# Performance work log

Hardware: AMD Instinct MI355X
Metric: run time of the kernel (lower is better)

Reference implementation:

```python
import math
import jax, jax.numpy as jnp
import numpy as np

B, S, D, H = 4, 2048, 1024, 16
HD = D // H
EPS = 1e-5
NEG = 1e10


def setup_inputs() -> dict:
    key = jax.random.key(0)
    ks = jax.random.split(key, 6)
    std = 0.02
    return {
        "x": jax.random.normal(ks[0], (B, S, D), dtype=jnp.float32),
        "ln1_w": jnp.ones((D,), jnp.float32),
        "ln1_b": jnp.zeros((D,), jnp.float32),
        "W_attn": jax.random.normal(ks[1], (D, 3 * D), jnp.float32) * std,
        "b_attn": jnp.zeros((3 * D,), jnp.float32),
        "W_cproj": jax.random.normal(ks[2], (D, D), jnp.float32) * std,
        "b_cproj": jnp.zeros((D,), jnp.float32),
        "ln2_w": jnp.ones((D,), jnp.float32),
        "ln2_b": jnp.zeros((D,), jnp.float32),
        "W_fc": jax.random.normal(ks[3], (D, 4 * D), jnp.float32) * std,
        "b_fc": jnp.zeros((4 * D,), jnp.float32),
        "W_mproj": jax.random.normal(ks[4], (4 * D, D), jnp.float32) * std,
        "b_mproj": jnp.zeros((D,), jnp.float32),
    }


def _layernorm(x, w, b):
    u = jnp.mean(x, axis=-1, keepdims=True)
    s = jnp.mean((x - u) ** 2, axis=-1, keepdims=True)
    return w * ((x - u) / jnp.sqrt(s + EPS)) + b


def _gelu(x):
    return 0.5 * x * (1 + jnp.tanh(math.sqrt(2 / math.pi) * (x + 0.044715 * x ** 3)))


def _block(x, ln1_w, ln1_b, W_attn, b_attn, W_cproj, b_cproj,
           ln2_w, ln2_b, W_fc, b_fc, W_mproj, b_mproj):
    h = _layernorm(x, ln1_w, ln1_b)
    qkv = h @ W_attn + b_attn                       # [B,S,3D]
    q, k, v = jnp.split(qkv, 3, axis=-1)
    # split heads -> [B,H,S,hd]
    q = q.reshape(B, S, H, HD).transpose(0, 2, 1, 3)
    k = k.reshape(B, S, H, HD).transpose(0, 2, 1, 3)
    v = v.reshape(B, S, H, HD).transpose(0, 2, 1, 3)
    w = jnp.einsum('bhqd,bhkd->bhqk', q, k) / math.sqrt(HD)
    bias = jnp.tril(jnp.ones((S, S), jnp.float32))  # causal mask
    w = w * bias - NEG * (1 - bias)
    w = jax.nn.softmax(w, axis=-1)
    a = jnp.einsum('bhqk,bhkd->bhqd', w, v)
    a = a.transpose(0, 2, 1, 3).reshape(B, S, D)    # merge heads
    a = a @ W_cproj + b_cproj
    x = x + a                                        # residual
    m = _layernorm(x, ln2_w, ln2_b)
    m = _gelu(m @ W_fc + b_fc) @ W_mproj + b_mproj
    return x + m


def reference(x, ln1_w, ln1_b, W_attn, b_attn, W_cproj, b_cproj,
              ln2_w, ln2_b, W_fc, b_fc, W_mproj, b_mproj):
    return _block(x, ln1_w, ln1_b, W_attn, b_attn, W_cproj, b_cproj,
                  ln2_w, ln2_b, W_fc, b_fc, W_mproj, b_mproj)
```

## Files before the change

### kernel.cpp

```cpp
#include <hip/hip_runtime.h>
#include <hip/hip_bf16.h>
#include <math.h>


typedef __attribute__((ext_vector_type(8))) short short8;
typedef __attribute__((ext_vector_type(4))) float floatx4;

#define MFMA16(a, b, c) __builtin_amdgcn_mfma_f32_16x16x32_bf16((a), (b), (c), 0, 0, 0)

__device__ __forceinline__ short f2bf(float f) {
    union { float f; unsigned u; } a; a.f = f;
    unsigned r = a.u + 0x7fffu + ((a.u >> 16) & 1u);
    return (short)(r >> 16);
}

__device__ __forceinline__ float fexp2(float x) {
    return exp2f(x);
}

__device__ __forceinline__ float gelu_f(float x) {
    return 0.5f * x * (1.0f + tanhf(0.7978845608028654f * (x + 0.044715f * x * x * x)));
}

__device__ __forceinline__ void gload_lds16(const short* g, short* l) {
    __builtin_amdgcn_global_load_lds((const __attribute__((address_space(1))) void*)g,
                                     (__attribute__((address_space(3))) void*)l, 16, 0, 0);
}

__global__ void tcast_kernel(const float* __restrict__ W, short* __restrict__ Wt,
                             int K, int N) {
    __shared__ float tile[32][33];
    const int bx = blockIdx.x * 32;
    const int by = blockIdx.y * 32;
    const int tx = threadIdx.x;
    const int ty = threadIdx.y;
#pragma unroll
    for (int i = 0; i < 32; i += 8)
        tile[ty + i][tx] = W[(size_t)(by + ty + i) * N + bx + tx];
    __syncthreads();
#pragma unroll
    for (int i = 0; i < 32; i += 8)
        Wt[(size_t)(bx + ty + i) * K + by + tx] = f2bf(tile[tx][ty + i]);
}

__global__ __launch_bounds__(256) void ln_kernel(const float* __restrict__ x,
                                                 const float* __restrict__ w,
                                                 const float* __restrict__ b,
                                                 short* __restrict__ out) {
    const int row = blockIdx.x;
    const int t = threadIdx.x;
    const float4 v = ((const float4*)(x + (size_t)row * 1024))[t];
    float s = v.x + v.y + v.z + v.w;
    float s2 = v.x * v.x + v.y * v.y + v.z * v.z + v.w * v.w;
#pragma unroll
    for (int d = 32; d >= 1; d >>= 1) {
        s += __shfl_xor(s, d, 64);
        s2 += __shfl_xor(s2, d, 64);
    }
    __shared__ float red[8];
    const int wid = t >> 6, lane = t & 63;
    if (lane == 0) { red[wid * 2] = s; red[wid * 2 + 1] = s2; }
    __syncthreads();
    s = red[0] + red[2] + red[4] + red[6];
    s2 = red[1] + red[3] + red[5] + red[7];
    const float mean = s * (1.f / 1024.f);
    const float var = s2 * (1.f / 1024.f) - mean * mean;
    const float rstd = rsqrtf(var + 1e-5f);
    const float4 wv = ((const float4*)w)[t];
    const float4 bv = ((const float4*)b)[t];
    union { ushort4 u; short sa[4]; } ov;
    ov.sa[0] = f2bf(wv.x * ((v.x - mean) * rstd) + bv.x);
    ov.sa[1] = f2bf(wv.y * ((v.y - mean) * rstd) + bv.y);
    ov.sa[2] = f2bf(wv.z * ((v.z - mean) * rstd) + bv.z);
    ov.sa[3] = f2bf(wv.w * ((v.w - mean) * rstd) + bv.w);
    ((ushort4*)(out + (size_t)row * 1024))[t] = ov.u;
}

template <int EPI>
__global__ __launch_bounds__(256) void gemm_kernel(
    const short* __restrict__ A, const short* __restrict__ Bt,
    const float* __restrict__ bias, const float* __restrict__ res,
    void* __restrict__ Cout, int M, int N, int K) {
    __shared__ __align__(16) short As[128][32];
    __shared__ __align__(16) short Bs[128][32];

    const int tid = threadIdx.x;
    const int wid = tid >> 6;
    const int lane = tid & 63;
    const int quad = lane >> 4;
    const int l16 = lane & 15;
    const int wm = (wid >> 1) * 64;
    const int wn = (wid & 1) * 64;
    const int m0 = blockIdx.y * 128;
    const int n0 = blockIdx.x * 128;

    const int lr = lane >> 2;
    const int lc = (lane & 3) * 8;

    floatx4 acc[4][4] = {};

    const short* ga0 = A + (size_t)(m0 + wid * 16 + lr) * K + lc;
    const short* ga1 = A + (size_t)(m0 + 64 + wid * 16 + lr) * K + lc;
    const short* gb0 = Bt + (size_t)(n0 + wid * 16 + lr) * K + lc;
    const short* gb1 = Bt + (size_t)(n0 + 64 + wid * 16 + lr) * K + lc;
    short* lA0 = &As[wid * 16][0];
    short* lA1 = &As[64 + wid * 16][0];
    short* lB0 = &Bs[wid * 16][0];
    short* lB1 = &Bs[64 + wid * 16][0];

    for (int k0 = 0; k0 < K; k0 += 32) {
        gload_lds16(ga0 + k0, lA0);
        gload_lds16(ga1 + k0, lA1);
        gload_lds16(gb0 + k0, lB0);
        gload_lds16(gb1 + k0, lB1);
        __syncthreads();
        short8 af[4], bf[4];
#pragma unroll
        for (int mt = 0; mt < 4; mt++)
            af[mt] = *(const short8*)&As[wm + mt * 16 + l16][quad * 8];
#pragma unroll
        for (int nt = 0; nt < 4; nt++)
            bf[nt] = *(const short8*)&Bs[wn + nt * 16 + l16][quad * 8];
#pragma unroll
        for (int mt = 0; mt < 4; mt++)
#pragma unroll
            for (int nt = 0; nt < 4; nt++)
                acc[mt][nt] = MFMA16(af[mt], bf[nt], acc[mt][nt]);
        __syncthreads();
    }
#pragma unroll
    for (int nt = 0; nt < 4; nt++) {
        const int col = n0 + wn + nt * 16 + l16;
        const float bv = bias[col];
#pragma unroll
        for (int mt = 0; mt < 4; mt++) {
#pragma unroll
            for (int r = 0; r < 4; r++) {
                const int row = m0 + wm + mt * 16 + quad * 4 + r;
                const size_t idx = (size_t)row * N + col;
                float v = acc[mt][nt][r] + bv;
                if constexpr (EPI == 0) {
                    ((short*)Cout)[idx] = f2bf(v);
                } else if constexpr (EPI == 1) {
                    ((short*)Cout)[idx] = f2bf(gelu_f(v));
                } else {
                    ((float*)Cout)[idx] = v + res[idx];
                }
            }
        }
    }
}

__global__ __launch_bounds__(256) void attn_kernel(const short* __restrict__ qkv,
                                                   short* __restrict__ aout) {
    __shared__ __align__(16) short smem[9216];
    short* Ks = smem;
    short* Vs = smem + 64 * 72;

    const int tid = threadIdx.x;
    const int wid = tid >> 6;
    const int lane = tid & 63;
    const int quad = lane >> 4;
    const int l16 = lane & 15;

    const int qtile = 15 - blockIdx.y;
    const int q0 = qtile * 128;
    const int bh = blockIdx.x;
    const int b = bh >> 4;
    const int h = bh & 15;

    const short* base = qkv + (size_t)b * 2048 * 3072 + h * 64;
    const int qrow_base = q0 + wid * 32;

    short8 qf[2][2];
#pragma unroll
    for (int qt = 0; qt < 2; qt++)
#pragma unroll
        for (int ks = 0; ks < 2; ks++)
            qf[qt][ks] = *(const short8*)(base +
                (size_t)(qrow_base + qt * 16 + l16) * 3072 + ks * 32 + quad * 8);

    floatx4 o[4][2] = {};
    float mrow[2] = {-1e30f, -1e30f};
    float lrow[2] = {0.f, 0.f};
    const float SCL = 0.125f * 1.44269504f;

    const int nkt = qtile * 2 + 2;
    for (int kt = 0; kt < nkt; kt++) {
        const int kt0 = kt * 64;
        {
            const int r = tid >> 2;
            const int cg = (tid & 3) * 16;
            const short* krow = base + (size_t)(kt0 + r) * 3072 + 1024 + cg;
            const short* vrow = base + (size_t)(kt0 + r) * 3072 + 2048 + cg;
            *(uint4*)&Ks[r * 72 + cg] = ((const uint4*)krow)[0];
            *(uint4*)&Ks[r * 72 + cg + 8] = ((const uint4*)krow)[1];
            *(uint2*)&Vs[r * 68 + cg] = ((const uint2*)vrow)[0];
            *(uint2*)&Vs[r * 68 + cg + 4] = ((const uint2*)vrow)[1];
            *(uint2*)&Vs[r * 68 + cg + 8] = ((const uint2*)vrow)[2];
            *(uint2*)&Vs[r * 68 + cg + 12] = ((const uint2*)vrow)[3];
        }
        __syncthreads();
        if (kt0 <= qrow_base + 31) {
            floatx4 st[4][2] = {};
#pragma unroll
            for (int kti = 0; kti < 4; kti++) {
                const short8 kf0 = *(const short8*)&Ks[(kti * 16 + l16) * 72 + quad * 8];
                const short8 kf1 = *(const short8*)&Ks[(kti * 16 + l16) * 72 + 32 + quad * 8];
#pragma unroll
                for (int qt = 0; qt < 2; qt++) {
                    st[kti][qt] = MFMA16(kf0, qf[qt][0], st[kti][qt]);
                    st[kti][qt] = MFMA16(kf1, qf[qt][1], st[kti][qt]);
                }
            }
            const bool needmask = (kt0 + 63) > qrow_base;
            short8 pk[2][2];
#pragma unroll
            for (int qt = 0; qt < 2; qt++) {
                const int q = qrow_base + qt * 16 + l16;
#pragma unroll
                for (int kti = 0; kti < 4; kti++)
#pragma unroll
                    for (int r = 0; r < 4; r++) {
                        float v = st[kti][qt][r] * SCL;
                        if (needmask && (kt0 + kti * 16 + quad * 4 + r) > q) v = -1e30f;
                        st[kti][qt][r] = v;
                    }
                float mx = -1e30f;
#pragma unroll
                for (int kti = 0; kti < 4; kti++)
#pragma unroll
                    for (int r = 0; r < 4; r++) mx = fmaxf(mx, st[kti][qt][r]);
                mx = fmaxf(mx, __shfl_xor(mx, 16, 64));
                mx = fmaxf(mx, __shfl_xor(mx, 32, 64));
                const float mnew = fmaxf(mrow[qt], mx);
                const float alpha = fexp2(mrow[qt] - mnew);
                mrow[qt] = mnew;
                float ps = 0.f;
#pragma unroll
                for (int kti = 0; kti < 4; kti++)
#pragma unroll
                    for (int r = 0; r < 4; r++) {
                        const float p = fexp2(st[kti][qt][r] - mnew);
                        st[kti][qt][r] = p;
                        ps += p;
                    }
                ps += __shfl_xor(ps, 16, 64);
                ps += __shfl_xor(ps, 32, 64);
                lrow[qt] = lrow[qt] * alpha + ps;
#pragma unroll
                for (int dt = 0; dt < 4; dt++) o[dt][qt] *= alpha;
#pragma unroll
                for (int kti = 0; kti < 4; kti++)
#pragma unroll
                    for (int r = 0; r < 4; r++)
                        pk[kti >> 1][qt][(kti & 1) * 4 + r] = f2bf(st[kti][qt][r]);
            }
#pragma unroll
            for (int c = 0; c < 2; c++)
#pragma unroll
                for (int dt = 0; dt < 4; dt++) {
                    short8 vf;
#pragma unroll
                    for (int j = 0; j < 4; j++) {
                        vf[j]     = Vs[(c * 32 + quad * 4 + j) * 68 + dt * 16 + l16];
                        vf[4 + j] = Vs[(c * 32 + 16 + quad * 4 + j) * 68 + dt * 16 + l16];
                    }
                    o[dt][0] = MFMA16(vf, pk[c][0], o[dt][0]);
                    o[dt][1] = MFMA16(vf, pk[c][1], o[dt][1]);
                }
        }
        __syncthreads();
    }
    short* Ow = smem + wid * (32 * 72);
    const float rl0 = 1.0f / lrow[0];
    const float rl1 = 1.0f / lrow[1];
#pragma unroll
    for (int dt = 0; dt < 4; dt++)
#pragma unroll
        for (int r = 0; r < 4; r++) {
            Ow[(l16) * 72 + dt * 16 + quad * 4 + r] = f2bf(o[dt][0][r] * rl0);
            Ow[(16 + l16) * 72 + dt * 16 + quad * 4 + r] = f2bf(o[dt][1][r] * rl1);
        }
    __asm__ volatile("s_waitcnt lgkmcnt(0)" ::: "memory");
    {
        const int ql = lane >> 1;
        const int h2 = lane & 1;
        short* orow = aout + (size_t)(b * 2048 + q0 + wid * 32 + ql) * 1024 + h * 64 + h2 * 32;
#pragma unroll
        for (int s = 0; s < 4; s++)
            *(uint4*)(orow + s * 8) = *(const uint4*)&Ow[ql * 72 + h2 * 32 + s * 8];
    }
}

extern "C" void kernel_launch(void* const* d_in, const int* in_sizes, int n_in,
                              void* d_out, int out_size, void* d_ws, size_t ws_size,
                              hipStream_t stream) {
    const float* x       = (const float*)d_in[0];
    const float* ln1_w   = (const float*)d_in[1];
    const float* ln1_b   = (const float*)d_in[2];
    const float* W_attn  = (const float*)d_in[3];
    const float* b_attn  = (const float*)d_in[4];
    const float* W_cproj = (const float*)d_in[5];
    const float* b_cproj = (const float*)d_in[6];
    const float* ln2_w   = (const float*)d_in[7];
    const float* ln2_b   = (const float*)d_in[8];
    const float* W_fc    = (const float*)d_in[9];
    const float* b_fc    = (const float*)d_in[10];
    const float* W_mproj = (const float*)d_in[11];
    const float* b_mproj = (const float*)d_in[12];

    char* ws = (char*)d_ws;
    short* W1t  = (short*)(ws + 0);
    short* W2t  = (short*)(ws + 6291456);
    short* W3t  = (short*)(ws + 8388608);
    short* W4t  = (short*)(ws + 16777216);
    short* h    = (short*)(ws + 25165824);
    short* aout = (short*)(ws + 41943040);
    short* big  = (short*)(ws + 58720256);
    float* x2   = (float*)d_out;
    float* out  = (float*)d_out;

    dim3 tb(32, 8);
    hipLaunchKernelGGL(tcast_kernel, dim3(96, 32), tb, 0, stream, W_attn, W1t, 1024, 3072);
    hipLaunchKernelGGL(tcast_kernel, dim3(32, 32), tb, 0, stream, W_cproj, W2t, 1024, 1024);
    hipLaunchKernelGGL(tcast_kernel, dim3(128, 32), tb, 0, stream, W_fc, W3t, 1024, 4096);
    hipLaunchKernelGGL(tcast_kernel, dim3(32, 128), tb, 0, stream, W_mproj, W4t, 4096, 1024);

    hipLaunchKernelGGL(ln_kernel, dim3(8192), dim3(256), 0, stream, x, ln1_w, ln1_b, h);

    hipLaunchKernelGGL((gemm_kernel<0>), dim3(24, 64), dim3(256), 0, stream,
                       h, W1t, b_attn, (const float*)nullptr, (void*)big, 8192, 3072, 1024);

    hipLaunchKernelGGL(attn_kernel, dim3(64, 16), dim3(256), 0, stream, big, aout);

    hipLaunchKernelGGL((gemm_kernel<2>), dim3(8, 64), dim3(256), 0, stream,
                       aout, W2t, b_cproj, x, (void*)x2, 8192, 1024, 1024);

    hipLaunchKernelGGL(ln_kernel, dim3(8192), dim3(256), 0, stream, x2, ln2_w, ln2_b, h);

    hipLaunchKernelGGL((gemm_kernel<1>), dim3(32, 64), dim3(256), 0, stream,
                       h, W3t, b_fc, (const float*)nullptr, (void*)big, 8192, 4096, 1024);

    hipLaunchKernelGGL((gemm_kernel<2>), dim3(8, 64), dim3(256), 0, stream,
                       big, W4t, b_mproj, x2, (void*)out, 8192, 1024, 4096);
}
```

Measured before the change: 609.0 us.

## Split-K the MLP down-projection GEMM and cheapen the GELU epilogue

The final 4096-deep GEMM is split into two K halves across blockIdx.z, doubling the block count from 512 to 1024. Each half writes bf16 partial sums, and a new reduce kernel adds the partials, bias and residual. The GELU epilogue swaps tanhf for an exp2 plus hardware-reciprocal form to cut transcendental cost. Rounding the partial sums to bf16 lowers output precision, and the extra pass adds memory traffic.

```diff
diff --git a/kernel.cpp b/kernel.cpp
--- a/kernel.cpp
+++ b/kernel.cpp
@@ -14,12 +14,23 @@
     return (short)(r >> 16);
 }
 
-__device__ __forceinline__ float fexp2(float x) {
-    return exp2f(x);
+__device__ __forceinline__ float bf2f(unsigned short u) {
+    union { unsigned u; float f; } a; a.u = ((unsigned)u) << 16;
+    return a.f;
+}
+
+__device__ __forceinline__ float fast_rcp(float x) {
+#if defined(__HIP_DEVICE_COMPILE__)
+    return __builtin_amdgcn_rcpf(x);
+#else
+    return 1.0f / x;
+#endif
 }
 
 __device__ __forceinline__ float gelu_f(float x) {
-    return 0.5f * x * (1.0f + tanhf(0.7978845608028654f * (x + 0.044715f * x * x * x)));
+    const float u = x + 0.044715f * x * x * x;
+    const float t = exp2f(2.302118131f * u);
+    return x - x * fast_rcp(t + 1.0f);
 }
 
 __device__ __forceinline__ void gload_lds16(const short* g, short* l) {
@@ -76,11 +87,30 @@
     ((ushort4*)(out + (size_t)row * 1024))[t] = ov.u;
 }
 
+__global__ __launch_bounds__(256) void reduce_kernel(
+    const unsigned short* __restrict__ p0, const unsigned short* __restrict__ p1,
+    const float* __restrict__ bias, const float* __restrict__ res,
+    float* __restrict__ out) {
+    const int row = blockIdx.x;
+    const int t = threadIdx.x;
+    const size_t off = (size_t)row * 1024;
+    const ushort4 a = ((const ushort4*)(p0 + off))[t];
+    const ushort4 c = ((const ushort4*)(p1 + off))[t];
+    const float4 r = ((const float4*)(res + off))[t];
+    const float4 bv = ((const float4*)bias)[t];
+    float4 o;
+    o.x = bf2f(a.x) + bf2f(c.x) + bv.x + r.x;
+    o.y = bf2f(a.y) + bf2f(c.y) + bv.y + r.y;
+    o.z = bf2f(a.z) + bf2f(c.z) + bv.z + r.z;
+    o.w = bf2f(a.w) + bf2f(c.w) + bv.w + r.w;
+    ((float4*)(out + off))[t] = o;
+}
+
 template <int EPI>
 __global__ __launch_bounds__(256) void gemm_kernel(
     const short* __restrict__ A, const short* __restrict__ Bt,
     const float* __restrict__ bias, const float* __restrict__ res,
-    void* __restrict__ Cout, int M, int N, int K) {
+    void* __restrict__ Cout, int M, int N, int Klen, int lda, int ldb) {
     __shared__ __align__(16) short As[128][32];
     __shared__ __align__(16) short Bs[128][32];
 
@@ -93,22 +123,23 @@
     const int wn = (wid & 1) * 64;
     const int m0 = blockIdx.y * 128;
     const int n0 = blockIdx.x * 128;
+    const int kbase = blockIdx.z * Klen;
 
     const int lr = lane >> 2;
     const int lc = (lane & 3) * 8;
 
     floatx4 acc[4][4] = {};
 
-    const short* ga0 = A + (size_t)(m0 + wid * 16 + lr) * K + lc;
-    const short* ga1 = A + (size_t)(m0 + 64 + wid * 16 + lr) * K + lc;
-    const short* gb0 = Bt + (size_t)(n0 + wid * 16 + lr) * K + lc;
-    const short* gb1 = Bt + (size_t)(n0 + 64 + wid * 16 + lr) * K + lc;
+    const short* ga0 = A + (size_t)(m0 + wid * 16 + lr) * lda + kbase + lc;
+    const short* ga1 = A + (size_t)(m0 + 64 + wid * 16 + lr) * lda + kbase + lc;
+    const short* gb0 = Bt + (size_t)(n0 + wid * 16 + lr) * ldb + kbase + lc;
+    const short* gb1 = Bt + (size_t)(n0 + 64 + wid * 16 + lr) * ldb + kbase + lc;
     short* lA0 = &As[wid * 16][0];
     short* lA1 = &As[64 + wid * 16][0];
     short* lB0 = &Bs[wid * 16][0];
     short* lB1 = &Bs[64 + wid * 16][0];
 
-    for (int k0 = 0; k0 < K; k0 += 32) {
+    for (int k0 = 0; k0 < Klen; k0 += 32) {
         gload_lds16(ga0 + k0, lA0);
         gload_lds16(ga1 + k0, lA1);
         gload_lds16(gb0 + k0, lB0);
@@ -131,7 +162,7 @@
 #pragma unroll
     for (int nt = 0; nt < 4; nt++) {
         const int col = n0 + wn + nt * 16 + l16;
-        const float bv = bias[col];
+        const float bv = (EPI == 3) ? 0.f : bias[col];
 #pragma unroll
         for (int mt = 0; mt < 4; mt++) {
 #pragma unroll
@@ -143,8 +174,10 @@
                     ((short*)Cout)[idx] = f2bf(v);
                 } else if constexpr (EPI == 1) {
                     ((short*)Cout)[idx] = f2bf(gelu_f(v));
+                } else if constexpr (EPI == 2) {
+                    ((float*)Cout)[idx] = v + res[idx];
                 } else {
-                    ((float*)Cout)[idx] = v + res[idx];
+                    ((short*)Cout)[(size_t)blockIdx.z * M * N + idx] = f2bf(v);
                 }
             }
         }
@@ -234,14 +267,14 @@
                 mx = fmaxf(mx, __shfl_xor(mx, 16, 64));
                 mx = fmaxf(mx, __shfl_xor(mx, 32, 64));
                 const float mnew = fmaxf(mrow[qt], mx);
-                const float alpha = fexp2(mrow[qt] - mnew);
+                const float alpha = exp2f(mrow[qt] - mnew);
                 mrow[qt] = mnew;
                 float ps = 0.f;
 #pragma unroll
                 for (int kti = 0; kti < 4; kti++)
 #pragma unroll
                     for (int r = 0; r < 4; r++) {
-                        const float p = fexp2(st[kti][qt][r] - mnew);
+                        const float p = exp2f(st[kti][qt][r] - mnew);
                         st[kti][qt][r] = p;
                         ps += p;
                     }
@@ -318,6 +351,7 @@
     short* h    = (short*)(ws + 25165824);
     short* aout = (short*)(ws + 41943040);
     short* big  = (short*)(ws + 58720256);
+    short* pbuf = h;
     float* x2   = (float*)d_out;
     float* out  = (float*)d_out;
 
@@ -329,19 +363,28 @@
 
     hipLaunchKernelGGL(ln_kernel, dim3(8192), dim3(256), 0, stream, x, ln1_w, ln1_b, h);
 
-    hipLaunchKernelGGL((gemm_kernel<0>), dim3(24, 64), dim3(256), 0, stream,
-                       h, W1t, b_attn, (const float*)nullptr, (void*)big, 8192, 3072, 1024);
+    hipLaunchKernelGGL((gemm_kernel<0>), dim3(24, 64, 1), dim3(256), 0, stream,
+                       h, W1t, b_attn, (const float*)nullptr, (void*)big,
+                       8192, 3072, 1024, 1024, 1024);
 
     hipLaunchKernelGGL(attn_kernel, dim3(64, 16), dim3(256), 0, stream, big, aout);
 
-    hipLaunchKernelGGL((gemm_kernel<2>), dim3(8, 64), dim3(256), 0, stream,
-                       aout, W2t, b_cproj, x, (void*)x2, 8192, 1024, 1024);
+    hipLaunchKernelGGL((gemm_kernel<2>), dim3(8, 64, 1), dim3(256), 0, stream,
+                       aout, W2t, b_cproj, x, (void*)x2,
+                       8192, 1024, 1024, 1024, 1024);
 
     hipLaunchKernelGGL(ln_kernel, dim3(8192), dim3(256), 0, stream, x2, ln2_w, ln2_b, h);
 
-    hipLaunchKernelGGL((gemm_kernel<1>), dim3(32, 64), dim3(256), 0, stream,
-                       h, W3t, b_fc, (const float*)nullptr, (void*)big, 8192, 4096, 1024);
-
-    hipLaunchKernelGGL((gemm_kernel<2>), dim3(8, 64), dim3(256), 0, stream,
-                       big, W4t, b_mproj, x2, (void*)out, 8192, 1024, 4096);
-}
+    hipLaunchKernelGGL((gemm_kernel<1>), dim3(32, 64, 1), dim3(256), 0, stream,
+                       h, W3t, b_fc, (const float*)nullptr, (void*)big,
+                       8192, 4096, 1024, 1024, 1024);
+
+    hipLaunchKernelGGL((gemm_kernel<3>), dim3(8, 64, 2), dim3(256), 0, stream,
+                       big, W4t, (const float*)nullptr, (const float*)nullptr, (void*)pbuf,
+                       8192, 1024, 2048, 4096, 4096);
+
+    hipLaunchKernelGGL(reduce_kernel, dim3(8192), dim3(256), 0, stream,
+                       (const unsigned short*)pbuf,
+                       (const unsigned short*)(pbuf + (size_t)8192 * 1024),
+                       b_mproj, x2, out);
+}
```

Measured after the change: 609.1 us. Within noise of the previous version (+0.0%).
